# Performance work log

Hardware: AMD Instinct MI355X
Metric: run time of the kernel (lower is better)

## Reference

```python
import jax, jax.numpy as jnp
import numpy as np

B_SZ, L, D, N = 2, 2048, 1024, 16


def setup_inputs() -> dict:
    key = jax.random.key(0)
    ks = jax.random.split(key, 8)
    x = jax.random.normal(ks[0], (B_SZ, L, D), dtype=jnp.float32)
    # torch.nn.Linear params: weight [out, in], bias [out]; y = x @ W.T + b
    s1 = 1.0 / np.sqrt(D)
    W1 = jax.random.uniform(ks[1], (D, D), minval=-s1, maxval=s1, dtype=jnp.float32)
    b1 = jax.random.uniform(ks[2], (D,), minval=-s1, maxval=s1, dtype=jnp.float32)
    W2 = jax.random.uniform(ks[3], (N, D), minval=-s1, maxval=s1, dtype=jnp.float32)
    b2 = jax.random.uniform(ks[4], (N,), minval=-s1, maxval=s1, dtype=jnp.float32)
    W3 = jax.random.uniform(ks[5], (N, D), minval=-s1, maxval=s1, dtype=jnp.float32)
    b3 = jax.random.uniform(ks[6], (N,), minval=-s1, maxval=s1, dtype=jnp.float32)
    # A: xavier_uniform on (D, N)
    lim = np.sqrt(6.0 / (D + N))
    A = jax.random.uniform(ks[7], (D, N), minval=-lim, maxval=lim, dtype=jnp.float32)
    return {"x": x, "W1": W1, "b1": b1, "W2": W2, "b2": b2, "W3": W3, "b3": b3, "A": A}


def reference(x, W1, b1, W2, b2, W3, b3, A):
    # delta = softplus(fc1(x)); B = fc2(x); C = fc3(x)
    delta = jax.nn.softplus(x @ W1.T + b1)          # [b, l, d]
    Bm = x @ W2.T + b2                               # [b, l, n]
    Cm = x @ W3.T + b3                               # [b, l, n]
    # discretization: dB = einsum('bld,bln->bldn', delta, B)
    dB = jnp.einsum('bld,bln->bldn', delta, Bm)      # [b, l, d, n]
    # dA = exp(einsum('bld,dn->bldn', delta, A)) is computed in the source but
    # multiplies a zero-initialized h, so it does not affect the output.
    # h = dA*0 + x[..., None] * dB
    h = x[..., None] * dB                            # [b, l, d, n]
    y = jnp.einsum('bln,bldn->bld', Cm, h)           # [b, l, d]
    return y
```

## Files before the change

kernel.cpp:

```cpp
#include <hip/hip_runtime.h>
#include <hip/hip_bf16.h>
#include <math.h>


typedef __bf16 bf16x8 __attribute__((ext_vector_type(8)));
typedef __bf16 bf16x4 __attribute__((ext_vector_type(4)));
typedef float  f32x4  __attribute__((ext_vector_type(4)));

#define MDIM 4096
#define KDIM 1024
#define NDIM 1024

__device__ __forceinline__ void async16(const void* g, void* l) {
    __builtin_amdgcn_global_load_lds(
        (const __attribute__((address_space(1))) void*)g,
        (__attribute__((address_space(3))) void*)l, 16, 0, 0);
}

__device__ __forceinline__ float softplus_f(float z) {
    return fmaxf(z, 0.f) + log1pf(__expf(-fabsf(z)));
}

__global__ __launch_bounds__(256)
void prep_kernel(const float* __restrict__ x, const float* __restrict__ W1,
                 const float* __restrict__ W2, const float* __restrict__ b2,
                 const float* __restrict__ W3, const float* __restrict__ b3,
                 __bf16* __restrict__ xb, __bf16* __restrict__ w1b,
                 float* __restrict__ s) {
    __shared__ __align__(16) __bf16 xs[16 * 1032];
    __shared__ __align__(16) __bf16 wq[4][32 * 264];
    __shared__ float red[4][2][16][16];
    const int t = threadIdx.x;
    const int wave = t >> 6, lane = t & 63;
    const int lrow = lane & 15, quad = lane >> 4;
    const size_t m0 = (size_t)blockIdx.x * 16;
    const int wk0 = wave * 256;

    {
        const float4* src = reinterpret_cast<const float4*>(W1) + (size_t)blockIdx.x * 1024;
        bf16x4* dst = reinterpret_cast<bf16x4*>(w1b) + (size_t)blockIdx.x * 1024;
#pragma unroll
        for (int i = 0; i < 4; ++i) {
            float4 v = src[i * 256 + t];
            bf16x4 h = { (__bf16)v.x, (__bf16)v.y, (__bf16)v.z, (__bf16)v.w };
            dst[i * 256 + t] = h;
        }
    }

#pragma unroll
    for (int i = 0; i < 16; ++i) {
        float4 v = *reinterpret_cast<const float4*>(x + (m0 + i) * KDIM + t * 4);
        bf16x4 h = { (__bf16)v.x, (__bf16)v.y, (__bf16)v.z, (__bf16)v.w };
        *reinterpret_cast<bf16x4*>(&xs[i * 1032 + t * 4]) = h;
        *reinterpret_cast<bf16x4*>(xb + (m0 + i) * KDIM + t * 4) = h;
    }

    {
        const int r16  = lane >> 2;
        const int cseg = (lane & 3) * 64;
#pragma unroll
        for (int j = 0; j < 8; ++j) {
            const int col = cseg + j * 8;
            const float* p2 = W2 + (size_t)r16 * KDIM + wk0 + col;
            float4 a0 = *reinterpret_cast<const float4*>(p2);
            float4 a1 = *reinterpret_cast<const float4*>(p2 + 4);
            bf16x8 h2 = { (__bf16)a0.x, (__bf16)a0.y, (__bf16)a0.z, (__bf16)a0.w,
                          (__bf16)a1.x, (__bf16)a1.y, (__bf16)a1.z, (__bf16)a1.w };
            *reinterpret_cast<bf16x8*>(&wq[wave][r16 * 264 + col]) = h2;
            const float* p3 = W3 + (size_t)r16 * KDIM + wk0 + col;
            float4 c0 = *reinterpret_cast<const float4*>(p3);
            float4 c1 = *reinterpret_cast<const float4*>(p3 + 4);
            bf16x8 h3 = { (__bf16)c0.x, (__bf16)c0.y, (__bf16)c0.z, (__bf16)c0.w,
                          (__bf16)c1.x, (__bf16)c1.y, (__bf16)c1.z, (__bf16)c1.w };
            *reinterpret_cast<bf16x8*>(&wq[wave][(16 + r16) * 264 + col]) = h3;
        }
    }
    __syncthreads();

    f32x4 acc[2] = {};
#pragma unroll
    for (int ks = 0; ks < 256; ks += 32) {
        bf16x8 a = *reinterpret_cast<const bf16x8*>(
            &xs[lrow * 1032 + wk0 + ks + quad * 8]);
        bf16x8 b0 = *reinterpret_cast<const bf16x8*>(
            &wq[wave][lrow * 264 + ks + quad * 8]);
        acc[0] = __builtin_amdgcn_mfma_f32_16x16x32_bf16(a, b0, acc[0], 0, 0, 0);
        bf16x8 b1 = *reinterpret_cast<const bf16x8*>(
            &wq[wave][(16 + lrow) * 264 + ks + quad * 8]);
        acc[1] = __builtin_amdgcn_mfma_f32_16x16x32_bf16(a, b1, acc[1], 0, 0, 0);
    }
#pragma unroll
    for (int r = 0; r < 4; ++r) {
        red[wave][0][quad * 4 + r][lrow] = acc[0][r];
        red[wave][1][quad * 4 + r][lrow] = acc[1][r];
    }
    __syncthreads();

    {
        const int row = t >> 4, n = t & 15;
        float Bv = red[0][0][row][n] + red[1][0][row][n]
                 + red[2][0][row][n] + red[3][0][row][n] + b2[n];
        float Cv = red[0][1][row][n] + red[1][1][row][n]
                 + red[2][1][row][n] + red[3][1][row][n] + b3[n];
        float p = Bv * Cv;
        p += __shfl_xor(p, 1);
        p += __shfl_xor(p, 2);
        p += __shfl_xor(p, 4);
        p += __shfl_xor(p, 8);
        if (n == 0) s[m0 + row] = p;
    }
}

#define GBM 128
#define GBN 64
#define GBK 128
__global__ __launch_bounds__(256, 2)
void gemm_bf(const __bf16* __restrict__ xb, const __bf16* __restrict__ w1b,
             const float* __restrict__ x, const float* __restrict__ b1,
             const float* __restrict__ s, float* __restrict__ y) {
    __shared__ __align__(16) __bf16 As[GBM * GBK];
    __shared__ __align__(16) __bf16 Bs[GBN * GBK];
    const int bm = blockIdx.y, bn = blockIdx.x;
    const int t = threadIdx.x;
    const int wave = t >> 6, lane = t & 63;
    const int wm = (wave >> 1) * 64, wn = (wave & 1) * 32;
    const int lrow = lane & 15, quad = lane >> 4;
    const int sr  = lane >> 4;
    const int pcg = lane & 15;
    const size_t m0 = (size_t)bm * GBM, n0 = (size_t)bn * GBN;

    f32x4 acc[4][2] = {};

    for (int k0 = 0; k0 < KDIM; k0 += GBK) {
#pragma unroll
        for (int i = 0; i < 8; ++i) {
            int q = i * 4 + wave;
            int row = q * 4 + sr;
            int lcg = pcg ^ (row & 15);
            async16(xb + (m0 + row) * KDIM + k0 + lcg * 8, &As[q * 512]);
        }
#pragma unroll
        for (int i = 0; i < 4; ++i) {
            int q = i * 4 + wave;
            int row = q * 4 + sr;
            int lcg = pcg ^ (row & 15);
            async16(w1b + (n0 + row) * KDIM + k0 + lcg * 8, &Bs[q * 512]);
        }
        __syncthreads();

#pragma unroll
        for (int kk = 0; kk < GBK; kk += 32) {
            const int cg = (kk >> 3) + quad;
            bf16x8 af[4], bfr[2];
#pragma unroll
            for (int mi = 0; mi < 4; ++mi) {
                int row = wm + mi * 16 + lrow;
                af[mi] = *reinterpret_cast<const bf16x8*>(
                    &As[row * GBK + ((cg ^ (row & 15)) << 3)]);
            }
#pragma unroll
            for (int ni = 0; ni < 2; ++ni) {
                int row = wn + ni * 16 + lrow;
                bfr[ni] = *reinterpret_cast<const bf16x8*>(
                    &Bs[row * GBK + ((cg ^ (row & 15)) << 3)]);
            }
#pragma unroll
            for (int mi = 0; mi < 4; ++mi)
#pragma unroll
                for (int ni = 0; ni < 2; ++ni)
                    acc[mi][ni] = __builtin_amdgcn_mfma_f32_16x16x32_bf16(
                        af[mi], bfr[ni], acc[mi][ni], 0, 0, 0);
        }
        __syncthreads();
    }

#pragma unroll
    for (int ni = 0; ni < 2; ++ni) {
        const size_t gn = n0 + wn + ni * 16 + lrow;
        const float bias = b1[gn];
#pragma unroll
        for (int mi = 0; mi < 4; ++mi) {
#pragma unroll
            for (int r = 0; r < 4; ++r) {
                const size_t gm = m0 + wm + mi * 16 + quad * 4 + r;
                float z = acc[mi][ni][r] + bias;
                y[gm * NDIM + gn] = x[gm * NDIM + gn] * softplus_f(z) * s[gm];
            }
        }
    }
}

__global__ __launch_bounds__(256)
void s_kernel_fb(const float* __restrict__ x,
                 const float* __restrict__ W2, const float* __restrict__ b2,
                 const float* __restrict__ W3, const float* __restrict__ b3,
                 float* __restrict__ s) {
    __shared__ float xs[1024];
    __shared__ float ps[8][32];
    __shared__ float bc[32];
    const int m = blockIdx.x;
    const int t = threadIdx.x;
    reinterpret_cast<float4*>(xs)[t] =
        reinterpret_cast<const float4*>(x + (size_t)m * 1024)[t];
    __syncthreads();
    const int n = t & 15;
    const int mat = (t >> 4) & 1;
    const int seg = t >> 5;
    const float* __restrict__ W = mat ? W3 : W2;
    const float* __restrict__ wr = W + (size_t)n * 1024 + seg * 128;
    const float* __restrict__ xr = xs + seg * 128;
    float p = 0.f;
#pragma unroll
    for (int i = 0; i < 128; i += 4) {
        float4 w4 = *reinterpret_cast<const float4*>(wr + i);
        float4 x4 = *reinterpret_cast<const float4*>(xr + i);
        p += w4.x * x4.x + w4.y * x4.y + w4.z * x4.z + w4.w * x4.w;
    }
    ps[seg][t & 31] = p;
    __syncthreads();
    if (t < 32) {
        float tot = 0.f;
#pragma unroll
        for (int g = 0; g < 8; ++g) tot += ps[g][t];
        tot += (t < 16) ? b2[t] : b3[t - 16];
        bc[t] = tot;
    }
    __syncthreads();
    if (t == 0) {
        float ss = 0.f;
#pragma unroll
        for (int nn = 0; nn < 16; ++nn) ss += bc[nn] * bc[16 + nn];
        s[m] = ss;
    }
}

#define BM 128
#define BN 64
#define BK 64
#define LDK 72
__global__ __launch_bounds__(256)
void gemm_fused_fb(const float* __restrict__ x, const float* __restrict__ W1,
                   const float* __restrict__ b1, const float* __restrict__ s,
                   float* __restrict__ y) {
    __shared__ __align__(16) __bf16 As[BM * LDK];
    __shared__ __align__(16) __bf16 Bs[BN * LDK];
    const int bm = blockIdx.y;
    const int bn = blockIdx.x;
    const int t = threadIdx.x;
    const int wave = t >> 6;
    const int lane = t & 63;
    const int wm = (wave >> 1) * 64;
    const int wn = (wave & 1) * 32;
    const int lrow = lane & 15;
    const int quad = lane >> 4;
    f32x4 acc[4][2] = {};
    const int rbase = t >> 4;
    const int scol = (t & 15) * 4;
    const float* __restrict__ xg = x + (size_t)(bm * BM) * KDIM + scol;
    const float* __restrict__ wg = W1 + (size_t)(bn * BN) * KDIM + scol;
    for (int k0 = 0; k0 < KDIM; k0 += BK) {
#pragma unroll
        for (int rr = 0; rr < 8; ++rr) {
            int row = rr * 16 + rbase;
            float4 v = *reinterpret_cast<const float4*>(xg + (size_t)row * KDIM + k0);
            bf16x4 h = { (__bf16)v.x, (__bf16)v.y, (__bf16)v.z, (__bf16)v.w };
            *reinterpret_cast<bf16x4*>(&As[row * LDK + scol]) = h;
        }
#pragma unroll
        for (int rr = 0; rr < 4; ++rr) {
            int row = rr * 16 + rbase;
            float4 v = *reinterpret_cast<const float4*>(wg + (size_t)row * KDIM + k0);
            bf16x4 h = { (__bf16)v.x, (__bf16)v.y, (__bf16)v.z, (__bf16)v.w };
            *reinterpret_cast<bf16x4*>(&Bs[row * LDK + scol]) = h;
        }
        __syncthreads();
#pragma unroll
        for (int kk = 0; kk < BK; kk += 32) {
            bf16x8 af[4];
            bf16x8 bfr[2];
#pragma unroll
            for (int mi = 0; mi < 4; ++mi)
                af[mi] = *reinterpret_cast<const bf16x8*>(
                    &As[(wm + mi * 16 + lrow) * LDK + kk + quad * 8]);
#pragma unroll
            for (int ni = 0; ni < 2; ++ni)
                bfr[ni] = *reinterpret_cast<const bf16x8*>(
                    &Bs[(wn + ni * 16 + lrow) * LDK + kk + quad * 8]);
#pragma unroll
            for (int mi = 0; mi < 4; ++mi)
#pragma unroll
                for (int ni = 0; ni < 2; ++ni)
                    acc[mi][ni] = __builtin_amdgcn_mfma_f32_16x16x32_bf16(
                        af[mi], bfr[ni], acc[mi][ni], 0, 0, 0);
        }
        __syncthreads();
    }
    const int gmb = bm * BM + wm;
    const int gnb = bn * BN + wn;
#pragma unroll
    for (int ni = 0; ni < 2; ++ni) {
        const int gn = gnb + ni * 16 + lrow;
        const float bias = b1[gn];
#pragma unroll
        for (int mi = 0; mi < 4; ++mi) {
            const int gm0 = gmb + mi * 16 + quad * 4;
#pragma unroll
            for (int r = 0; r < 4; ++r) {
                const int gm = gm0 + r;
                float z = acc[mi][ni][r] + bias;
                y[(size_t)gm * NDIM + gn] =
                    x[(size_t)gm * NDIM + gn] * softplus_f(z) * s[gm];
            }
        }
    }
}

extern "C" void kernel_launch(void* const* d_in, const int* in_sizes, int n_in,
                              void* d_out, int out_size, void* d_ws, size_t ws_size,
                              hipStream_t stream) {
    const float* x  = (const float*)d_in[0];
    const float* W1 = (const float*)d_in[1];
    const float* b1 = (const float*)d_in[2];
    const float* W2 = (const float*)d_in[3];
    const float* b2 = (const float*)d_in[4];
    const float* W3 = (const float*)d_in[5];
    const float* b3 = (const float*)d_in[6];

    float* y = (float*)d_out;

    const size_t XB_BYTES = (size_t)MDIM * KDIM * 2;
    const size_t WB_BYTES = (size_t)NDIM * KDIM * 2;
    const size_t S_BYTES  = (size_t)MDIM * 4;

    if (ws_size >= XB_BYTES + WB_BYTES + S_BYTES) {
        __bf16* xb  = (__bf16*)d_ws;
        __bf16* w1b = (__bf16*)((char*)d_ws + XB_BYTES);
        float*  s   = (float*)((char*)d_ws + XB_BYTES + WB_BYTES);
        prep_kernel<<<dim3(MDIM / 16), dim3(256), 0, stream>>>(
            x, W1, W2, b2, W3, b3, xb, w1b, s);
        gemm_bf<<<dim3(NDIM / GBN, MDIM / GBM), dim3(256), 0, stream>>>(
            xb, w1b, x, b1, s, y);
    } else {
        float* s = (float*)d_ws;
        s_kernel_fb<<<dim3(MDIM), dim3(256), 0, stream>>>(x, W2, b2, W3, b3, s);
        gemm_fused_fb<<<dim3(NDIM / BN, MDIM / BM), dim3(256), 0, stream>>>(x, W1, b1, s, y);
    }
}
```

Measured before the change: 115.2 us.

## Load W2/W3 directly into MFMA operands and shrink GEMM tile to 64x64

The prep kernel no longer stages the W2/W3 bf16 copies in shared memory. Each wave now reads its fp32 weight slices straight from global memory and converts them in registers before the MFMA, which removes a large LDS buffer and one staging pass. The main GEMM tile drops from 128x64 to 64x64 with launch bounds allowing 4 blocks per CU, so there are twice as many blocks and occupancy is higher, but each block reuses its loaded data less. The A and B async loads are merged into a single loop.

```diff
diff --git a/kernel.cpp b/kernel.cpp
--- a/kernel.cpp
+++ b/kernel.cpp
@@ -21,14 +21,19 @@
     return fmaxf(z, 0.f) + log1pf(__expf(-fabsf(z)));
 }
 
+__device__ __forceinline__ bf16x8 cvt8(float4 v0, float4 v1) {
+    bf16x8 h = { (__bf16)v0.x, (__bf16)v0.y, (__bf16)v0.z, (__bf16)v0.w,
+                 (__bf16)v1.x, (__bf16)v1.y, (__bf16)v1.z, (__bf16)v1.w };
+    return h;
+}
+
 __global__ __launch_bounds__(256)
-void prep_kernel(const float* __restrict__ x, const float* __restrict__ W1,
-                 const float* __restrict__ W2, const float* __restrict__ b2,
-                 const float* __restrict__ W3, const float* __restrict__ b3,
-                 __bf16* __restrict__ xb, __bf16* __restrict__ w1b,
-                 float* __restrict__ s) {
+void prep2(const float* __restrict__ x, const float* __restrict__ W1,
+           const float* __restrict__ W2, const float* __restrict__ b2,
+           const float* __restrict__ W3, const float* __restrict__ b3,
+           __bf16* __restrict__ xb, __bf16* __restrict__ w1b,
+           float* __restrict__ s) {
     __shared__ __align__(16) __bf16 xs[16 * 1032];
-    __shared__ __align__(16) __bf16 wq[4][32 * 264];
     __shared__ float red[4][2][16][16];
     const int t = threadIdx.x;
     const int wave = t >> 6, lane = t & 63;
@@ -54,27 +59,6 @@
         *reinterpret_cast<bf16x4*>(&xs[i * 1032 + t * 4]) = h;
         *reinterpret_cast<bf16x4*>(xb + (m0 + i) * KDIM + t * 4) = h;
     }
-
-    {
-        const int r16  = lane >> 2;
-        const int cseg = (lane & 3) * 64;
-#pragma unroll
-        for (int j = 0; j < 8; ++j) {
-            const int col = cseg + j * 8;
-            const float* p2 = W2 + (size_t)r16 * KDIM + wk0 + col;
-            float4 a0 = *reinterpret_cast<const float4*>(p2);
-            float4 a1 = *reinterpret_cast<const float4*>(p2 + 4);
-            bf16x8 h2 = { (__bf16)a0.x, (__bf16)a0.y, (__bf16)a0.z, (__bf16)a0.w,
-                          (__bf16)a1.x, (__bf16)a1.y, (__bf16)a1.z, (__bf16)a1.w };
-            *reinterpret_cast<bf16x8*>(&wq[wave][r16 * 264 + col]) = h2;
-            const float* p3 = W3 + (size_t)r16 * KDIM + wk0 + col;
-            float4 c0 = *reinterpret_cast<const float4*>(p3);
-            float4 c1 = *reinterpret_cast<const float4*>(p3 + 4);
-            bf16x8 h3 = { (__bf16)c0.x, (__bf16)c0.y, (__bf16)c0.z, (__bf16)c0.w,
-                          (__bf16)c1.x, (__bf16)c1.y, (__bf16)c1.z, (__bf16)c1.w };
-            *reinterpret_cast<bf16x8*>(&wq[wave][(16 + r16) * 264 + col]) = h3;
-        }
-    }
     __syncthreads();
 
     f32x4 acc[2] = {};
@@ -82,12 +66,18 @@
     for (int ks = 0; ks < 256; ks += 32) {
         bf16x8 a = *reinterpret_cast<const bf16x8*>(
             &xs[lrow * 1032 + wk0 + ks + quad * 8]);
-        bf16x8 b0 = *reinterpret_cast<const bf16x8*>(
-            &wq[wave][lrow * 264 + ks + quad * 8]);
-        acc[0] = __builtin_amdgcn_mfma_f32_16x16x32_bf16(a, b0, acc[0], 0, 0, 0);
-        bf16x8 b1 = *reinterpret_cast<const bf16x8*>(
-            &wq[wave][(16 + lrow) * 264 + ks + quad * 8]);
-        acc[1] = __builtin_amdgcn_mfma_f32_16x16x32_bf16(a, b1, acc[1], 0, 0, 0);
+        {
+            const float* p2 = W2 + (size_t)lrow * KDIM + wk0 + ks + quad * 8;
+            float4 v0 = *reinterpret_cast<const float4*>(p2);
+            float4 v1 = *reinterpret_cast<const float4*>(p2 + 4);
+            acc[0] = __builtin_amdgcn_mfma_f32_16x16x32_bf16(a, cvt8(v0, v1), acc[0], 0, 0, 0);
+        }
+        {
+            const float* p3 = W3 + (size_t)lrow * KDIM + wk0 + ks + quad * 8;
+            float4 v0 = *reinterpret_cast<const float4*>(p3);
+            float4 v1 = *reinterpret_cast<const float4*>(p3 + 4);
+            acc[1] = __builtin_amdgcn_mfma_f32_16x16x32_bf16(a, cvt8(v0, v1), acc[1], 0, 0, 0);
+        }
     }
 #pragma unroll
     for (int r = 0; r < 4; ++r) {
@@ -111,10 +101,10 @@
     }
 }
 
-#define GBM 128
+#define GBM 64
 #define GBN 64
 #define GBK 128
-__global__ __launch_bounds__(256, 2)
+__global__ __launch_bounds__(256, 4)
 void gemm_bf(const __bf16* __restrict__ xb, const __bf16* __restrict__ w1b,
              const float* __restrict__ x, const float* __restrict__ b1,
              const float* __restrict__ s, float* __restrict__ y) {
@@ -123,27 +113,21 @@
     const int bm = blockIdx.y, bn = blockIdx.x;
     const int t = threadIdx.x;
     const int wave = t >> 6, lane = t & 63;
-    const int wm = (wave >> 1) * 64, wn = (wave & 1) * 32;
+    const int wm = (wave >> 1) * 32, wn = (wave & 1) * 32;
     const int lrow = lane & 15, quad = lane >> 4;
     const int sr  = lane >> 4;
     const int pcg = lane & 15;
     const size_t m0 = (size_t)bm * GBM, n0 = (size_t)bn * GBN;
 
-    f32x4 acc[4][2] = {};
+    f32x4 acc[2][2] = {};
 
     for (int k0 = 0; k0 < KDIM; k0 += GBK) {
 #pragma unroll
-        for (int i = 0; i < 8; ++i) {
-            int q = i * 4 + wave;
+        for (int i = 0; i < 4; ++i) {
+            int q = wave * 4 + i;
             int row = q * 4 + sr;
             int lcg = pcg ^ (row & 15);
             async16(xb + (m0 + row) * KDIM + k0 + lcg * 8, &As[q * 512]);
-        }
-#pragma unroll
-        for (int i = 0; i < 4; ++i) {
-            int q = i * 4 + wave;
-            int row = q * 4 + sr;
-            int lcg = pcg ^ (row & 15);
             async16(w1b + (n0 + row) * KDIM + k0 + lcg * 8, &Bs[q * 512]);
         }
         __syncthreads();
@@ -151,9 +135,9 @@
 #pragma unroll
         for (int kk = 0; kk < GBK; kk += 32) {
             const int cg = (kk >> 3) + quad;
-            bf16x8 af[4], bfr[2];
-#pragma unroll
-            for (int mi = 0; mi < 4; ++mi) {
+            bf16x8 af[2], bfr[2];
+#pragma unroll
+            for (int mi = 0; mi < 2; ++mi) {
                 int row = wm + mi * 16 + lrow;
                 af[mi] = *reinterpret_cast<const bf16x8*>(
                     &As[row * GBK + ((cg ^ (row & 15)) << 3)]);
@@ -165,7 +149,7 @@
                     &Bs[row * GBK + ((cg ^ (row & 15)) << 3)]);
             }
 #pragma unroll
-            for (int mi = 0; mi < 4; ++mi)
+            for (int mi = 0; mi < 2; ++mi)
 #pragma unroll
                 for (int ni = 0; ni < 2; ++ni)
                     acc[mi][ni] = __builtin_amdgcn_mfma_f32_16x16x32_bf16(
@@ -179,7 +163,7 @@
         const size_t gn = n0 + wn + ni * 16 + lrow;
         const float bias = b1[gn];
 #pragma unroll
-        for (int mi = 0; mi < 4; ++mi) {
+        for (int mi = 0; mi < 2; ++mi) {
 #pragma unroll
             for (int r = 0; r < 4; ++r) {
                 const size_t gm = m0 + wm + mi * 16 + quad * 4 + r;
@@ -336,7 +320,7 @@
         __bf16* xb  = (__bf16*)d_ws;
         __bf16* w1b = (__bf16*)((char*)d_ws + XB_BYTES);
         float*  s   = (float*)((char*)d_ws + XB_BYTES + WB_BYTES);
-        prep_kernel<<<dim3(MDIM / 16), dim3(256), 0, stream>>>(
+        prep2<<<dim3(MDIM / 16), dim3(256), 0, stream>>>(
             x, W1, W2, b2, W3, b3, xb, w1b, s);
         gemm_bf<<<dim3(NDIM / GBN, MDIM / GBM), dim3(256), 0, stream>>>(
             xb, w1b, x, b1, s, y);
```

Measured after the change: 111.1 us. 3.5% less time.
